# Kernel tuning notes

Measured on AMD Instinct MI355X. Metric: run time of the kernel, lower is better.

The kernel has to match this reference:

```python
import jax, jax.numpy as jnp
import numpy as np

B, T, SD = 16, 512, 64          # batch, action seq len, sample_dim
EMB, HD = 1024, 64              # emb_dim, head_dim
NH = EMB // HD                  # 16 heads
DEPTH, NREG, LAT, FF = 8, 16, 256, 4 * EMB
S = T + NREG                    # total sequence length (actions + registers)


def setup_inputs() -> dict:
    key = jax.random.key(0)
    ks = jax.random.split(key, 16)
    def n(k, shape, scale=0.02):
        return jax.random.normal(k, shape, jnp.float32) * scale
    return {
        "sample": jax.random.normal(ks[0], (B, T, SD), jnp.float32),
        "W_emb": n(ks[1], (SD, EMB)), "b_emb": jnp.zeros((EMB,), jnp.float32),
        "pos": n(ks[2], (T, EMB)),
        "registers": n(ks[3], (NREG, EMB), 1.0),
        "ln1_s": jnp.ones((DEPTH, EMB), jnp.float32), "ln1_b": jnp.zeros((DEPTH, EMB), jnp.float32),
        "W_qkv": n(ks[4], (DEPTH, EMB, 3 * EMB)), "b_qkv": jnp.zeros((DEPTH, 3 * EMB), jnp.float32),
        "W_o": n(ks[5], (DEPTH, EMB, EMB)), "b_o": jnp.zeros((DEPTH, EMB), jnp.float32),
        "ln2_s": jnp.ones((DEPTH, EMB), jnp.float32), "ln2_b": jnp.zeros((DEPTH, EMB), jnp.float32),
        "W_fc1": n(ks[6], (DEPTH, EMB, FF)), "b_fc1": jnp.zeros((DEPTH, FF), jnp.float32),
        "W_fc2": n(ks[7], (DEPTH, FF, EMB)), "b_fc2": jnp.zeros((DEPTH, EMB), jnp.float32),
        "lnf_s": jnp.ones((EMB,), jnp.float32), "lnf_b": jnp.zeros((EMB,), jnp.float32),
        "W_head": n(ks[8], (EMB, LAT)), "b_head": jnp.zeros((LAT,), jnp.float32),
    }


def _ln(x, s, b):
    m = jnp.mean(x, -1, keepdims=True)
    v = jnp.var(x, -1, keepdims=True)
    return (x - m) * jax.lax.rsqrt(v + 1e-5) * s + b


def _causal_last_mask():
    # True = attended to. Actions attend to all actions but NOT registers;
    # registers attend to all actions and causally (incl. self) to registers.
    allowed = jnp.ones((S, S), jnp.bool_)
    allowed = allowed.at[:T, T:].set(False)
    allowed = allowed.at[T:, T:].set(jnp.tril(jnp.ones((NREG, NREG), jnp.bool_)))
    return allowed


def reference(sample, W_emb, b_emb, pos, registers, ln1_s, ln1_b, W_qkv, b_qkv,
              W_o, b_o, ln2_s, ln2_b, W_fc1, b_fc1, W_fc2, b_fc2,
              lnf_s, lnf_b, W_head, b_head):
    # embed + positional add
    x = sample @ W_emb + b_emb + pos[None, :, :]          # [B,T,E]
    # concat registers
    x = jnp.concatenate([x, jnp.broadcast_to(registers, (B, NREG, EMB))], axis=1)  # [B,S,E]
    mask = _causal_last_mask()                             # [S,S]
    scale = 1.0 / jnp.sqrt(jnp.asarray(HD, x.dtype))
    for i in range(DEPTH):
        # pre-LN multi-head attention with structured block mask
        h = _ln(x, ln1_s[i], ln1_b[i])
        qkv = h @ W_qkv[i] + b_qkv[i]
        q, k, v = jnp.split(qkv, 3, axis=-1)
        q = q.reshape(B, S, NH, HD)
        k = k.reshape(B, S, NH, HD)
        v = v.reshape(B, S, NH, HD)
        att = jnp.einsum('bqhd,bkhd->bhqk', q, k) * scale
        att = jnp.where(mask[None, None], att, jnp.finfo(att.dtype).min)
        att = jax.nn.softmax(att, axis=-1)
        o = jnp.einsum('bhqk,bkhd->bqhd', att, v).reshape(B, S, EMB)
        x = x + o @ W_o[i] + b_o[i]
        # pre-LN MLP
        h2 = _ln(x, ln2_s[i], ln2_b[i])
        x = x + jax.nn.gelu(h2 @ W_fc1[i] + b_fc1[i]) @ W_fc2[i] + b_fc2[i]
    x = _ln(x, lnf_s, lnf_b)
    # head applied to register positions only
    return x[:, T:] @ W_head + b_head                      # [B,NREG,LAT]
```

## Files before the change

### kernel.cpp

```cpp
#include <hip/hip_runtime.h>
#include <hip/hip_bf16.h>


typedef unsigned short u16;
typedef __attribute__((ext_vector_type(4))) float f32x4;
typedef __attribute__((ext_vector_type(8))) __bf16 bf16x8;

#define DEV static __device__ __forceinline__

constexpr int Bb = 16, Tt = 512, E = 1024, HD = 64, NHd = 16;
constexpr int DEPTH = 8, NREG = 16, LAT = 256, FF = 4096;
constexpr int S = Tt + NREG;
constexpr int SPAD = 576;
constexpr int MR = Bb * S;
constexpr int ME = Bb * Tt;

DEV u16 f2bf(float f) {
  unsigned u = __builtin_bit_cast(unsigned, f);
  u += 0x7fffu + ((u >> 16) & 1u);
  return (u16)(u >> 16);
}

DEV void gll16(const u16* g, u16* l) {
  __builtin_amdgcn_global_load_lds((const __attribute__((address_space(1))) void*)g,
                                   (__attribute__((address_space(3))) void*)l, 16, 0, 0);
}

enum { M_EMBED, M_QKV, M_OPROJ, M_FC1, M_FC2, M_HEAD };

struct GA {
  const u16* A; const u16* Bt;
  int K, lda, ldb, Nrows, ldc;
  const float* bias; const float* pos;
  float* fout; u16* bout;
  u16 *qp, *kp, *vtp;
};

template<int MODE, int BN>
__global__ __launch_bounds__(256)
void gemm_bt(GA g) {
  constexpr int NI = BN / 32;
  __shared__ __align__(16) u16 As[3][128 * 32];
  __shared__ __align__(16) u16 Bs[3][BN * 32];
  const int tid = threadIdx.x;
  const u16* A  = g.A;
  const u16* Bt = g.Bt;

  int tM, tN;
  {
    const int nwg = gridDim.x * gridDim.y;
    int flat = blockIdx.y * gridDim.x + blockIdx.x;
    const int q = nwg >> 3, r = nwg & 7;
    const int xcd = flat & 7, loc = flat >> 3;
    flat = (xcd < r ? xcd * (q + 1) : r * (q + 1) + (xcd - r) * q) + loc;
    tM = flat / gridDim.x; tN = flat % gridDim.x;
  }

  const int lane = tid & 63, wid = tid >> 6;
  const int wr = wid >> 1, wc = wid & 1;
  const int fr = lane & 15, fg = lane >> 4;

  const int arow = tM * 128 + (tid >> 2);
  int br0 = tN * BN + (tid >> 2);
  if (br0 > g.Nrows - 1) br0 = g.Nrows - 1;
  int br1 = tN * BN + 64 + (tid >> 2);
  if (br1 > g.Nrows - 1) br1 = g.Nrows - 1;
  const int kseg = ((tid & 3) ^ ((tid >> 3) & 3)) * 8;
  const int woff = (tid & 192) * 8;

  const u16* ag0 = A  + (long)arow        * g.lda + kseg;
  const u16* ag1 = A  + (long)(arow + 64) * g.lda + kseg;
  const u16* bg0 = Bt + (long)br0         * g.ldb + kseg;
  const u16* bg1 = Bt + (long)br1         * g.ldb + kseg;

  f32x4 acc[4][NI];
#pragma unroll
  for (int i = 0; i < 4; ++i)
#pragma unroll
    for (int j = 0; j < NI; ++j) acc[i][j] = f32x4{0.f, 0.f, 0.f, 0.f};

#define STAGE(KT, BUF) do {                                   \
    const int _k0 = (KT) << 5;                                \
    gll16(ag0 + _k0, &As[BUF][woff]);                         \
    gll16(ag1 + _k0, &As[BUF][woff + 2048]);                  \
    gll16(bg0 + _k0, &Bs[BUF][woff]);                         \
    if (BN == 128) gll16(bg1 + _k0, &Bs[BUF][woff + 2048]);   \
  } while (0)

  const int nk = g.K >> 5;
  STAGE(0, 0);
  if (nk > 1) STAGE(1, 1);

  const int rsw = (fg ^ ((fr >> 1) & 3)) * 8;
  constexpr int LPS = (BN == 128) ? 4 : 3;

  for (int kt = 0; kt < nk; ++kt) {
    const int cur = kt % 3;
    if (kt < nk - 1) {
      asm volatile("s_waitcnt vmcnt(%0)" :: "i"(LPS) : "memory");
    } else {
      asm volatile("s_waitcnt vmcnt(0)" ::: "memory");
    }
    __builtin_amdgcn_sched_barrier(0);
    __builtin_amdgcn_s_barrier();
    __builtin_amdgcn_sched_barrier(0);
    if (kt + 2 < nk) STAGE(kt + 2, (kt + 2) % 3);

    bf16x8 af[4], bfr[NI];
#pragma unroll
    for (int mi = 0; mi < 4; ++mi)
      af[mi] = *(const bf16x8*)&As[cur][(wr * 64 + mi * 16 + fr) * 32 + rsw];
#pragma unroll
    for (int ni = 0; ni < NI; ++ni)
      bfr[ni] = *(const bf16x8*)&Bs[cur][(wc * (BN / 2) + ni * 16 + fr) * 32 + rsw];
    __builtin_amdgcn_s_setprio(1);
#pragma unroll
    for (int mi = 0; mi < 4; ++mi)
#pragma unroll
      for (int ni = 0; ni < NI; ++ni)
        acc[mi][ni] = __builtin_amdgcn_mfma_f32_16x16x32_bf16(af[mi], bfr[ni], acc[mi][ni], 0, 0, 0);
    __builtin_amdgcn_s_setprio(0);
  }
#undef STAGE

#pragma unroll
  for (int mi = 0; mi < 4; ++mi)
#pragma unroll
    for (int ni = 0; ni < NI; ++ni)
#pragma unroll
      for (int j = 0; j < 4; ++j) {
        const int row = tM * 128 + wr * 64 + mi * 16 + fg * 4 + j;
        const int col = tN * BN + wc * (BN / 2) + ni * 16 + fr;
        float v = acc[mi][ni][j];
        if (MODE == M_EMBED) {
          const int b = row >> 9, t = row & 511;
          v += g.bias[col] + g.pos[(long)t * E + col];
          g.fout[((long)(b * S + t)) * E + col] = v;
        } else if (MODE == M_QKV) {
          const int b = row / S, s = row - b * S;
          v += g.bias[col];
          const int part = col >> 10, c = col & 1023;
          const int hh = c >> 6, d = c & 63;
          const u16 bf = f2bf(v);
          if (part == 0)      g.qp [((long)((b * NHd + hh) * SPAD + s)) * HD + d] = bf;
          else if (part == 1) g.kp [((long)((b * NHd + hh) * SPAD + s)) * HD + d] = bf;
          else                g.vtp[((long)((b * NHd + hh) * HD   + d)) * SPAD + s] = bf;
        } else if (MODE == M_OPROJ || MODE == M_FC2) {
          const long idx = (long)row * g.ldc + col;
          g.fout[idx] += v + g.bias[col];
        } else if (MODE == M_FC1) {
          v += g.bias[col];
          const float z = 0.7978845608028654f * (v + 0.044715f * v * v * v);
          const float e = __expf(2.f * z);
          const float th = 1.f - 2.f / (e + 1.f);
          g.bout[(long)row * g.ldc + col] = f2bf(0.5f * v * (1.f + th));
        } else if (MODE == M_HEAD) {
          g.fout[(long)row * g.ldc + col] = v + g.bias[col];
        }
      }
}

__global__ __launch_bounds__(256)
void flash_k(const u16* __restrict__ q, const u16* __restrict__ k,
             const u16* __restrict__ vt, u16* __restrict__ o) {
  __shared__ __align__(16) u16 Ks[2][64 * 64];
  __shared__ __align__(16) u16 Vs[2][64 * 64];
  __shared__ __align__(16) u16 Ps[4 * 16 * 64];
  const int tid = threadIdx.x;
  const int lane = tid & 63, w = tid >> 6;
  const int fr = lane & 15, fg = lane >> 4;

  int flat = blockIdx.y * 9 + blockIdx.x;
  flat = (flat & 7) * 288 + (flat >> 3);
  const int bh = flat / 9, qt = flat % 9;
  const int q0 = qt * 64;

  const u16* qrow = q + ((long)bh * SPAD + q0 + w * 16 + fr) * HD;
  const bf16x8 qf0 = *(const bf16x8*)(qrow + fg * 8);
  const bf16x8 qf1 = *(const bf16x8*)(qrow + 32 + fg * 8);

  const int srow = lane >> 3;
  const int sseg = (((lane & 7) ^ (srow & 7)) * 8);
  const u16* kg = k  + ((long)bh * SPAD + w * 16 + srow) * HD + sseg;
  const u16* vg = vt + ((long)(bh * HD + w * 16 + srow)) * SPAD + sseg;

#define STAGE_F(KT, BUF) do {                                       \
    gll16(kg + (KT) * 64 * HD,          &Ks[BUF][w * 16 * HD]);     \
    gll16(kg + (KT) * 64 * HD + 8 * HD, &Ks[BUF][w * 16 * HD + 8 * HD]); \
    gll16(vg + (KT) * 64,               &Vs[BUF][w * 16 * HD]);     \
    gll16(vg + (KT) * 64 + 8 * SPAD,    &Vs[BUF][w * 16 * HD + 8 * HD]); \
  } while (0)

  const int frm = fr & 7;

  float m[4], lsum[4]; f32x4 oa[4];
#pragma unroll
  for (int j = 0; j < 4; ++j) { m[j] = -1e30f; lsum[j] = 0.f; }
#pragma unroll
  for (int n = 0; n < 4; ++n) oa[n] = f32x4{0.f, 0.f, 0.f, 0.f};

  const int nt = (q0 < Tt) ? 8 : 9;
  STAGE_F(0, 0);
  for (int kt = 0; kt < nt; ++kt) {
    const int cur = kt & 1;
    asm volatile("s_waitcnt vmcnt(0)" ::: "memory");
    __builtin_amdgcn_sched_barrier(0);
    __builtin_amdgcn_s_barrier();
    __builtin_amdgcn_sched_barrier(0);
    if (kt + 1 < nt) STAGE_F(kt + 1, cur ^ 1);

    f32x4 sfr[4];
#pragma unroll
    for (int n = 0; n < 4; ++n) {
      const bf16x8 kf0 = *(const bf16x8*)&Ks[cur][(n * 16 + fr) * HD + ((fg ^ frm) * 8)];
      const bf16x8 kf1 = *(const bf16x8*)&Ks[cur][(n * 16 + fr) * HD + (((fg + 4) ^ frm) * 8)];
      sfr[n] = __builtin_amdgcn_mfma_f32_16x16x32_bf16(qf0, kf0, f32x4{0.f,0.f,0.f,0.f}, 0, 0, 0);
      sfr[n] = __builtin_amdgcn_mfma_f32_16x16x32_bf16(qf1, kf1, sfr[n], 0, 0, 0);
    }
    float p[4][4];
#pragma unroll
    for (int j = 0; j < 4; ++j) {
      const int qg = q0 + w * 16 + fg * 4 + j;
      const int vlim = qg < Tt ? Tt : qg + 1;
#pragma unroll
      for (int n = 0; n < 4; ++n) {
        const int col = kt * 64 + n * 16 + fr;
        p[n][j] = (col < vlim) ? sfr[n][j] * 0.125f : -1e30f;
      }
    }
#pragma unroll
    for (int j = 0; j < 4; ++j) {
      float pm = fmaxf(fmaxf(p[0][j], p[1][j]), fmaxf(p[2][j], p[3][j]));
#pragma unroll
      for (int msk = 1; msk <= 8; msk <<= 1) pm = fmaxf(pm, __shfl_xor(pm, msk));
      const float mn = fmaxf(m[j], pm);
      const float corr = __expf(m[j] - mn);
      m[j] = mn;
      float rs = 0.f;
#pragma unroll
      for (int n = 0; n < 4; ++n) { const float e = __expf(p[n][j] - mn); p[n][j] = e; rs += e; }
#pragma unroll
      for (int msk = 1; msk <= 8; msk <<= 1) rs += __shfl_xor(rs, msk);
      lsum[j] = lsum[j] * corr + rs;
#pragma unroll
      for (int n = 0; n < 4; ++n) oa[n][j] *= corr;
    }
#pragma unroll
    for (int j = 0; j < 4; ++j) {
      const int r = fg * 4 + j;
#pragma unroll
      for (int n = 0; n < 4; ++n) {
        const int gr = 2 * n + (fr >> 3);
        Ps[w * 1024 + r * 64 + ((gr ^ (r & 7)) * 8) + frm] = f2bf(p[n][j]);
      }
    }
    asm volatile("s_waitcnt lgkmcnt(0)" ::: "memory");
    __builtin_amdgcn_sched_barrier(0);
    const bf16x8 pf0 = *(const bf16x8*)&Ps[w * 1024 + fr * 64 + ((fg ^ frm) * 8)];
    const bf16x8 pf1 = *(const bf16x8*)&Ps[w * 1024 + fr * 64 + (((fg + 4) ^ frm) * 8)];
#pragma unroll
    for (int n = 0; n < 4; ++n) {
      const bf16x8 vf0 = *(const bf16x8*)&Vs[cur][(n * 16 + fr) * HD + ((fg ^ frm) * 8)];
      const bf16x8 vf1 = *(const bf16x8*)&Vs[cur][(n * 16 + fr) * HD + (((fg + 4) ^ frm) * 8)];
      oa[n] = __builtin_amdgcn_mfma_f32_16x16x32_bf16(pf0, vf0, oa[n], 0, 0, 0);
      oa[n] = __builtin_amdgcn_mfma_f32_16x16x32_bf16(pf1, vf1, oa[n], 0, 0, 0);
    }
  }
#undef STAGE_F

  const int b = bh >> 4, hh = bh & 15;
#pragma unroll
  for (int j = 0; j < 4; ++j) {
    const int qg = q0 + w * 16 + fg * 4 + j;
    if (qg < S) {
      const float inv = 1.f / lsum[j];
#pragma unroll
      for (int n = 0; n < 4; ++n)
        o[((long)(b * S + qg)) * E + hh * HD + n * 16 + fr] = f2bf(oa[n][j] * inv);
    }
  }
}

__global__ __launch_bounds__(256)
void ln_k(const float* __restrict__ x, const float* __restrict__ sc,
          const float* __restrict__ bi, u16* __restrict__ out, int gather) {
  const int r = blockIdx.x;
  const int srow = gather ? ((r >> 4) * S + Tt + (r & 15)) : r;
  const float4 v = ((const float4*)(x + (long)srow * E))[threadIdx.x];
  float s = v.x + v.y + v.z + v.w;
  float q = v.x * v.x + v.y * v.y + v.z * v.z + v.w * v.w;
#pragma unroll
  for (int o = 32; o; o >>= 1) { s += __shfl_down(s, o); q += __shfl_down(q, o); }
  __shared__ float ps[8];
  if ((threadIdx.x & 63) == 0) { ps[threadIdx.x >> 6] = s; ps[4 + (threadIdx.x >> 6)] = q; }
  __syncthreads();
  s = ps[0] + ps[1] + ps[2] + ps[3];
  q = ps[4] + ps[5] + ps[6] + ps[7];
  const float mean = s * (1.f / E);
  const float rs = rsqrtf(q * (1.f / E) - mean * mean + 1e-5f);
  const int c = threadIdx.x * 4;
  ushort4 o4;
  o4.x = f2bf((v.x - mean) * rs * sc[c + 0] + bi[c + 0]);
  o4.y = f2bf((v.y - mean) * rs * sc[c + 1] + bi[c + 1]);
  o4.z = f2bf((v.z - mean) * rs * sc[c + 2] + bi[c + 2]);
  o4.w = f2bf((v.w - mean) * rs * sc[c + 3] + bi[c + 3]);
  ((ushort4*)(out + (long)r * E))[threadIdx.x] = o4;
}

__global__ __launch_bounds__(256)
void wtrans(const float* __restrict__ src, u16* __restrict__ dst, int R, int C) {
  __shared__ float t[32][33];
  const int c0 = blockIdx.x * 32, r0 = blockIdx.y * 32;
  const int tx = threadIdx.x & 31, ty = threadIdx.x >> 5;
#pragma unroll
  for (int i = 0; i < 32; i += 8) t[ty + i][tx] = src[(long)(r0 + ty + i) * C + c0 + tx];
  __syncthreads();
#pragma unroll
  for (int i = 0; i < 32; i += 8) dst[(long)(c0 + ty + i) * R + r0 + tx] = f2bf(t[tx][ty + i]);
}

__global__ void cvt_bf(const float* __restrict__ in, u16* __restrict__ out, long n) {
  const long i = ((long)blockIdx.x * blockDim.x + threadIdx.x) * 4;
  if (i >= n) return;
  const float4 v = *(const float4*)(in + i);
  ushort4 o; o.x = f2bf(v.x); o.y = f2bf(v.y); o.z = f2bf(v.z); o.w = f2bf(v.w);
  *(ushort4*)(out + i) = o;
}

__global__ void zero_k(float4* p, long n) {
  long i = (long)blockIdx.x * blockDim.x + threadIdx.x;
  const long st = (long)gridDim.x * blockDim.x;
  const float4 z = make_float4(0.f, 0.f, 0.f, 0.f);
  for (; i < n; i += st) p[i] = z;
}

__global__ void reg_copy(const float* __restrict__ regs, float* __restrict__ x) {
  const int b = blockIdx.x >> 4, r = blockIdx.x & 15;
  const float4* sp = (const float4*)(regs + (long)r * E);
  float4* dp = (float4*)(x + ((long)(b * S + Tt + r)) * E);
  dp[threadIdx.x] = sp[threadIdx.x];
}

constexpr long OFF_WQKV = 0L;
constexpr long OFF_WO   = OFF_WQKV + 3072L * 1024 * 2;
constexpr long OFF_WFC1 = OFF_WO   + 1024L * 1024 * 2;
constexpr long OFF_WFC2 = OFF_WFC1 + 4096L * 1024 * 2;
constexpr long OFF_WEMB = OFF_WFC2 + 1024L * 4096 * 2;
constexpr long OFF_WHEAD= OFF_WEMB + 1024L * 64 * 2;
constexpr long OFF_SMP  = OFF_WHEAD+ 256L * 1024 * 2;
constexpr long OFF_X    = OFF_SMP  + (long)ME * 64 * 2;
constexpr long OFF_H    = OFF_X    + (long)MR * E * 4;
constexpr long OFF_Q    = OFF_H    + (long)MR * E * 2;
constexpr long OFF_K    = OFF_Q    + 256L * SPAD * HD * 2;
constexpr long OFF_VT   = OFF_K    + 256L * SPAD * HD * 2;
constexpr long OFF_O    = OFF_VT   + 256L * SPAD * HD * 2;
constexpr long OFF_HF   = OFF_O    + (long)MR * FF * 2;
constexpr long WS_NEED  = OFF_HF   + 256L * 1024 * 2;

extern "C" void kernel_launch(void* const* d_in, const int* in_sizes, int n_in,
                              void* d_out, int out_size, void* d_ws, size_t ws_size,
                              hipStream_t stream) {
  if (ws_size < (size_t)WS_NEED) return;

  const float* sample = (const float*)d_in[0];
  const float* W_emb  = (const float*)d_in[1];
  const float* b_emb  = (const float*)d_in[2];
  const float* pos    = (const float*)d_in[3];
  const float* regs   = (const float*)d_in[4];
  const float* ln1_s  = (const float*)d_in[5];
  const float* ln1_b  = (const float*)d_in[6];
  const float* W_qkv  = (const float*)d_in[7];
  const float* b_qkv  = (const float*)d_in[8];
  const float* W_o    = (const float*)d_in[9];
  const float* b_o    = (const float*)d_in[10];
  const float* ln2_s  = (const float*)d_in[11];
  const float* ln2_b  = (const float*)d_in[12];
  const float* W_fc1  = (const float*)d_in[13];
  const float* b_fc1  = (const float*)d_in[14];
  const float* W_fc2  = (const float*)d_in[15];
  const float* b_fc2  = (const float*)d_in[16];
  const float* lnf_s  = (const float*)d_in[17];
  const float* lnf_b  = (const float*)d_in[18];
  const float* W_head = (const float*)d_in[19];
  const float* b_head = (const float*)d_in[20];

  char* w = (char*)d_ws;
  u16* wqkvT = (u16*)(w + OFF_WQKV);
  u16* woT   = (u16*)(w + OFF_WO);
  u16* wfc1T = (u16*)(w + OFF_WFC1);
  u16* wfc2T = (u16*)(w + OFF_WFC2);
  u16* wembT = (u16*)(w + OFF_WEMB);
  u16* wheadT= (u16*)(w + OFF_WHEAD);
  u16* smp   = (u16*)(w + OFF_SMP);
  float* x   = (float*)(w + OFF_X);
  u16* h     = (u16*)(w + OFF_H);
  u16* qp    = (u16*)(w + OFF_Q);
  u16* kp    = (u16*)(w + OFF_K);
  u16* vtp   = (u16*)(w + OFF_VT);
  u16* o     = (u16*)(w + OFF_O);
  u16* a1    = (u16*)(w + OFF_O);
  u16* hf    = (u16*)(w + OFF_HF);

  wtrans<<<dim3(32, 2, 1), 256, 0, stream>>>(W_emb,  wembT, 64, 1024);
  wtrans<<<dim3(8, 32, 1), 256, 0, stream>>>(W_head, wheadT, 1024, 256);
  cvt_bf<<<dim3(512), 256, 0, stream>>>(sample, smp, (long)ME * 64);
  zero_k<<<dim3(2048), 256, 0, stream>>>((float4*)qp, (3L * 256 * SPAD * HD * 2) / 16);

  {
    GA g{}; g.A = smp; g.Bt = wembT; g.K = 64; g.lda = 64; g.ldb = 64;
    g.Nrows = E; g.bias = b_emb; g.pos = pos; g.fout = x;
    gemm_bt<M_EMBED, 64><<<dim3(16, 64, 1), 256, 0, stream>>>(g);
  }
  reg_copy<<<dim3(256), 256, 0, stream>>>(regs, x);

  for (int L = 0; L < DEPTH; ++L) {
    wtrans<<<dim3(96, 32, 1),  256, 0, stream>>>(W_qkv + (long)L * 1024 * 3072, wqkvT, 1024, 3072);
    wtrans<<<dim3(32, 32, 1),  256, 0, stream>>>(W_o   + (long)L * 1024 * 1024, woT,   1024, 1024);
    wtrans<<<dim3(128, 32, 1), 256, 0, stream>>>(W_fc1 + (long)L * 1024 * 4096, wfc1T, 1024, 4096);
    wtrans<<<dim3(32, 128, 1), 256, 0, stream>>>(W_fc2 + (long)L * 4096 * 1024, wfc2T, 4096, 1024);

    ln_k<<<dim3(MR), 256, 0, stream>>>(x, ln1_s + L * E, ln1_b + L * E, h, 0);
    {
      GA g{}; g.A = h; g.Bt = wqkvT;
      g.K = 1024; g.lda = 1024; g.ldb = 1024; g.Nrows = 3072;
      g.bias = b_qkv + L * 3072; g.qp = qp; g.kp = kp; g.vtp = vtp;
      gemm_bt<M_QKV, 128><<<dim3(24, 66, 1), 256, 0, stream>>>(g);
    }
    flash_k<<<dim3(9, 256, 1), 256, 0, stream>>>(qp, kp, vtp, o);
    {
      GA g{}; g.A = o; g.Bt = woT;
      g.K = 1024; g.lda = 1024; g.ldb = 1024; g.Nrows = 1024; g.ldc = 1024;
      g.bias = b_o + L * E; g.fout = x;
      gemm_bt<M_OPROJ, 64><<<dim3(16, 66, 1), 256, 0, stream>>>(g);
    }
    ln_k<<<dim3(MR), 256, 0, stream>>>(x, ln2_s + L * E, ln2_b + L * E, h, 0);
    {
      GA g{}; g.A = h; g.Bt = wfc1T;
      g.K = 1024; g.lda = 1024; g.ldb = 1024; g.Nrows = 4096; g.ldc = 4096;
      g.bias = b_fc1 + L * FF; g.bout = a1;
      gemm_bt<M_FC1, 128><<<dim3(32, 66, 1), 256, 0, stream>>>(g);
    }
    {
      GA g{}; g.A = a1; g.Bt = wfc2T;
      g.K = 4096; g.lda = 4096; g.ldb = 4096; g.Nrows = 1024; g.ldc = 1024;
      g.bias = b_fc2 + L * E; g.fout = x;
      gemm_bt<M_FC2, 64><<<dim3(16, 66, 1), 256, 0, stream>>>(g);
    }
  }

  ln_k<<<dim3(256), 256, 0, stream>>>(x, lnf_s, lnf_b, hf, 1);
  {
    GA g{}; g.A = hf; g.Bt = wheadT; g.K = 1024; g.lda = 1024; g.ldb = 1024;
    g.Nrows = LAT; g.ldc = LAT; g.bias = b_head; g.fout = (float*)d_out;
    gemm_bt<M_HEAD, 128><<<dim3(2, 2, 1), 256, 0, stream>>>(g);
  }
}
```

Baseline: 4.307 ms.

## Switch GEMM to BK=64 double-buffered pipeline and widen O-proj/FC2 tiles

The GEMM main loop now stages 64-wide K tiles in two LDS buffers instead of 32-wide tiles in three. Each wave loads its own row slab with an 8-way XOR swizzle, which halves the number of loop iterations and barriers per K. O-projection and FC2 now use 128-wide N tiles, so fewer, larger workgroups run. The Nrows clamp on B rows is gone, which risks out-of-range reads for the head GEMM with 256 rows. An extra barrier per iteration and shallower prefetch depth could expose more memory latency.

```diff
diff --git a/kernel.cpp b/kernel.cpp
--- a/kernel.cpp
+++ b/kernel.cpp
@@ -40,11 +40,10 @@
 __global__ __launch_bounds__(256)
 void gemm_bt(GA g) {
   constexpr int NI = BN / 32;
-  __shared__ __align__(16) u16 As[3][128 * 32];
-  __shared__ __align__(16) u16 Bs[3][BN * 32];
+  constexpr int LPS = 4 + NI;
+  __shared__ __align__(16) u16 As[2][128 * 64];
+  __shared__ __align__(16) u16 Bs[2][BN * 64];
   const int tid = threadIdx.x;
-  const u16* A  = g.A;
-  const u16* Bt = g.Bt;
 
   int tM, tN;
   {
@@ -60,18 +59,11 @@
   const int wr = wid >> 1, wc = wid & 1;
   const int fr = lane & 15, fg = lane >> 4;
 
-  const int arow = tM * 128 + (tid >> 2);
-  int br0 = tN * BN + (tid >> 2);
-  if (br0 > g.Nrows - 1) br0 = g.Nrows - 1;
-  int br1 = tN * BN + 64 + (tid >> 2);
-  if (br1 > g.Nrows - 1) br1 = g.Nrows - 1;
-  const int kseg = ((tid & 3) ^ ((tid >> 3) & 3)) * 8;
-  const int woff = (tid & 192) * 8;
-
-  const u16* ag0 = A  + (long)arow        * g.lda + kseg;
-  const u16* ag1 = A  + (long)(arow + 64) * g.lda + kseg;
-  const u16* bg0 = Bt + (long)br0         * g.ldb + kseg;
-  const u16* bg1 = Bt + (long)br1         * g.ldb + kseg;
+  const int skew = ((lane & 7) ^ ((lane >> 3) & 7)) * 8;
+  const int srA = tM * 128 + wid * 32 + (lane >> 3);
+  const int srB = tN * BN + wid * (BN / 4) + (lane >> 3);
+  const u16* ag = g.A  + (long)srA * g.lda + skew;
+  const u16* bg = g.Bt + (long)srB * g.ldb + skew;
 
   f32x4 acc[4][NI];
 #pragma unroll
@@ -79,24 +71,25 @@
 #pragma unroll
     for (int j = 0; j < NI; ++j) acc[i][j] = f32x4{0.f, 0.f, 0.f, 0.f};
 
-#define STAGE(KT, BUF) do {                                   \
-    const int _k0 = (KT) << 5;                                \
-    gll16(ag0 + _k0, &As[BUF][woff]);                         \
-    gll16(ag1 + _k0, &As[BUF][woff + 2048]);                  \
-    gll16(bg0 + _k0, &Bs[BUF][woff]);                         \
-    if (BN == 128) gll16(bg1 + _k0, &Bs[BUF][woff + 2048]);   \
+#define STAGE(KT, BUF) do {                                               \
+    const long _k0 = (long)(KT) * 64;                                     \
+    _Pragma("unroll")                                                     \
+    for (int i = 0; i < 4; ++i)                                           \
+      gll16(ag + (long)(8 * i) * g.lda + _k0, &As[BUF][wid * 2048 + i * 512]); \
+    _Pragma("unroll")                                                     \
+    for (int i = 0; i < NI; ++i)                                          \
+      gll16(bg + (long)(8 * i) * g.ldb + _k0, &Bs[BUF][wid * (BN / 4) * 64 + i * 512]); \
   } while (0)
 
-  const int nk = g.K >> 5;
+  const int nk = g.K >> 6;
   STAGE(0, 0);
-  if (nk > 1) STAGE(1, 1);
-
-  const int rsw = (fg ^ ((fr >> 1) & 3)) * 8;
-  constexpr int LPS = (BN == 128) ? 4 : 3;
+
+  const int rx = (fr & 7);
 
   for (int kt = 0; kt < nk; ++kt) {
-    const int cur = kt % 3;
-    if (kt < nk - 1) {
+    const int cur = kt & 1;
+    if (kt + 1 < nk) {
+      STAGE(kt + 1, cur ^ 1);
       asm volatile("s_waitcnt vmcnt(%0)" :: "i"(LPS) : "memory");
     } else {
       asm volatile("s_waitcnt vmcnt(0)" ::: "memory");
@@ -104,22 +97,31 @@
     __builtin_amdgcn_sched_barrier(0);
     __builtin_amdgcn_s_barrier();
     __builtin_amdgcn_sched_barrier(0);
-    if (kt + 2 < nk) STAGE(kt + 2, (kt + 2) % 3);
-
-    bf16x8 af[4], bfr[NI];
-#pragma unroll
-    for (int mi = 0; mi < 4; ++mi)
-      af[mi] = *(const bf16x8*)&As[cur][(wr * 64 + mi * 16 + fr) * 32 + rsw];
-#pragma unroll
-    for (int ni = 0; ni < NI; ++ni)
-      bfr[ni] = *(const bf16x8*)&Bs[cur][(wc * (BN / 2) + ni * 16 + fr) * 32 + rsw];
+
+    bf16x8 af[2][4], bfr[2][NI];
+#pragma unroll
+    for (int kk = 0; kk < 2; ++kk) {
+#pragma unroll
+      for (int mi = 0; mi < 4; ++mi)
+        af[kk][mi] = *(const bf16x8*)&As[cur][(wr * 64 + mi * 16 + fr) * 64 +
+                                             (((kk * 4 + fg) ^ rx) * 8)];
+#pragma unroll
+      for (int ni = 0; ni < NI; ++ni)
+        bfr[kk][ni] = *(const bf16x8*)&Bs[cur][(wc * (BN / 2) + ni * 16 + fr) * 64 +
+                                              (((kk * 4 + fg) ^ rx) * 8)];
+    }
     __builtin_amdgcn_s_setprio(1);
 #pragma unroll
-    for (int mi = 0; mi < 4; ++mi)
-#pragma unroll
-      for (int ni = 0; ni < NI; ++ni)
-        acc[mi][ni] = __builtin_amdgcn_mfma_f32_16x16x32_bf16(af[mi], bfr[ni], acc[mi][ni], 0, 0, 0);
+    for (int kk = 0; kk < 2; ++kk)
+#pragma unroll
+      for (int mi = 0; mi < 4; ++mi)
+#pragma unroll
+        for (int ni = 0; ni < NI; ++ni)
+          acc[mi][ni] = __builtin_amdgcn_mfma_f32_16x16x32_bf16(af[kk][mi], bfr[kk][ni],
+                                                                acc[mi][ni], 0, 0, 0);
     __builtin_amdgcn_s_setprio(0);
+    __builtin_amdgcn_sched_barrier(0);
+    __builtin_amdgcn_s_barrier();
   }
 #undef STAGE
 
@@ -431,7 +433,7 @@
       GA g{}; g.A = o; g.Bt = woT;
       g.K = 1024; g.lda = 1024; g.ldb = 1024; g.Nrows = 1024; g.ldc = 1024;
       g.bias = b_o + L * E; g.fout = x;
-      gemm_bt<M_OPROJ, 64><<<dim3(16, 66, 1), 256, 0, stream>>>(g);
+      gemm_bt<M_OPROJ, 128><<<dim3(8, 66, 1), 256, 0, stream>>>(g);
     }
     ln_k<<<dim3(MR), 256, 0, stream>>>(x, ln2_s + L * E, ln2_b + L * E, h, 0);
     {
@@ -444,7 +446,7 @@
       GA g{}; g.A = a1; g.Bt = wfc2T;
       g.K = 4096; g.lda = 4096; g.ldb = 4096; g.Nrows = 1024; g.ldc = 1024;
       g.bias = b_fc2 + L * E; g.fout = x;
-      gemm_bt<M_FC2, 64><<<dim3(16, 66, 1), 256, 0, stream>>>(g);
+      gemm_bt<M_FC2, 128><<<dim3(8, 66, 1), 256, 0, stream>>>(g);
     }
   }
 
```

New measurement: 4.336 ms. About the same (+0.7%).
